# Performance work log

Hardware: AMD Instinct MI355X
Metric: run time of the kernel (lower is better)

## Reference

```python
import jax, jax.numpy as jnp
import numpy as np

B, S, D = 64, 4096, 64          # bsz*n_heads, seq_len, head_size
WINDOW = 256                    # num_toks_attended
NEG = -10000.0


def setup_inputs() -> dict:
    key = jax.random.key(0)
    kq, kk, kv = jax.random.split(key, 3)
    q = jax.random.normal(kq, (B, S, D), dtype=jnp.float32)
    k = jax.random.normal(kk, (B, S, D), dtype=jnp.float32)
    v = jax.random.normal(kv, (B, S, D), dtype=jnp.float32)
    return {"q": q, "k": k, "v": v}


def reference(q, k, v):
    # sliding_window_attn, topk_for_softmax=-1 (plain softmax)
    b, s, d = q.shape
    hw = WINDOW // 2                       # half window = 128
    n = s // hw                            # number of half-window bins
    split = lambda x: x.reshape(b, n, hw, d)
    bq, bk, bv = split(q), split(k), split(v)

    def cat_half_neighbours(x):
        # left-rolled, self, right-rolled half-bins -> [b, n, 3*hw, d]
        return jnp.concatenate(
            (jnp.roll(x, 1, axis=1), x, jnp.roll(x, -1, axis=1)), axis=-2)

    bk = cat_half_neighbours(bk)
    bv = cat_half_neighbours(bv)

    dots = jnp.einsum('bnid,bnjd->bnij', bq, bk) * (d ** -0.5)  # [b,n,hw,3hw]

    # mask: strict lower triangle on left block, none on middle,
    # upper-incl-diagonal on right block (as in the torch code)
    lmask = jnp.tril(jnp.ones((hw, hw), dtype=bool), -1)
    mask = jnp.concatenate((lmask, jnp.zeros_like(lmask), ~lmask), axis=-1)
    dots = jnp.where(mask, NEG, dots)

    p = jax.nn.softmax(dots, axis=-1)
    bo = jnp.einsum('bnij,bnjd->bnid', p, bv)
    return bo.reshape(b, s, d)
```

## Files before the change

kernel.cpp:

```cpp
#include <hip/hip_runtime.h>
#include <hip/hip_bf16.h>
#include <stdint.h>

using f32x4  = __attribute__((ext_vector_type(4))) float;
using bf16x8 = __attribute__((ext_vector_type(8))) __bf16;
using bf16x2 = __attribute__((ext_vector_type(2))) __bf16;
typedef unsigned int u32;

#define SEQ  4096
#define NEGV -10000.0f

__global__ __launch_bounds__(256) void lattn_kern(
        const float* __restrict__ Q, const float* __restrict__ K,
        const float* __restrict__ V, float* __restrict__ O)
{
    __shared__ __bf16 Kl[320 * 64];
    __shared__ __bf16 Vt[64 * 320];

    const int tid  = threadIdx.x;
    const int wv   = tid >> 6;
    const int lane = tid & 63;
    const int g    = lane >> 4;
    const int c    = lane & 15;

    const int obid = blockIdx.x;
    const int bid  = (obid & 7) * 512 + (obid >> 3);
    const int b    = bid >> 6;
    const int tb   = bid & 63;
    const int t0   = tb * 64;

    const size_t baseB = (size_t)b * (SEQ * 64);

    #pragma unroll
    for (int i = 0; i < 10; ++i) {
        const int ch   = tid + i * 256;
        const int row  = ch >> 3;
        const int dg   = ch & 7;
        const int grow = (t0 - 128 + row) & (SEQ - 1);
        const float* src = K + baseB + (size_t)grow * 64 + dg * 8;
        f32x4 k0 = *(const f32x4*)(src);
        f32x4 k1 = *(const f32x4*)(src + 4);
        bf16x8 hk;
        #pragma unroll
        for (int u = 0; u < 4; ++u) { hk[u] = (__bf16)k0[u]; hk[u + 4] = (__bf16)k1[u]; }
        const u32 kb = (u32)row * 128u + (u32)((dg ^ (row & 7)) * 16);
        *(bf16x8*)((char*)Kl + kb) = hk;
    }

    #pragma unroll
    for (int i = 0; i < 5; ++i) {
        const int ch   = tid + i * 256;
        const int rp   = ch >> 3;
        const int dg   = ch & 7;
        const int grow = (t0 - 128 + 2 * rp) & (SEQ - 1);
        const float* src = V + baseB + (size_t)grow * 64 + dg * 8;
        f32x4 a0 = *(const f32x4*)(src);
        f32x4 a1 = *(const f32x4*)(src + 4);
        f32x4 b0 = *(const f32x4*)(src + 64);
        f32x4 b1 = *(const f32x4*)(src + 68);
        #pragma unroll
        for (int u = 0; u < 8; ++u) {
            const int d  = dg * 8 + u;
            const float lo = (u < 4) ? a0[u] : a1[u - 4];
            const float hi = (u < 4) ? b0[u] : b1[u - 4];
            bf16x2 pv; pv[0] = (__bf16)lo; pv[1] = (__bf16)hi;
            const u32 sw = (u32)(u ^ dg);
            const u32 vb = ((u32)d * 640u + (u32)rp * 4u) ^ (sw << 4);
            *(bf16x2*)((char*)Vt + vb) = pv;
        }
    }

    bf16x8 aq[2];
    {
        const float* qp = Q + baseB + (size_t)(t0 + wv * 16 + c) * 64 + g * 8;
        #pragma unroll
        for (int kk = 0; kk < 2; ++kk) {
            f32x4 q0 = *(const f32x4*)(qp + kk * 32);
            f32x4 q1 = *(const f32x4*)(qp + kk * 32 + 4);
            #pragma unroll
            for (int u = 0; u < 4; ++u) { aq[kk][u] = (__bf16)q0[u]; aq[kk][u + 4] = (__bf16)q1[u]; }
        }
    }

    __syncthreads();

    f32x4 s_[20];
    #pragma unroll
    for (int t = 0; t < 20; ++t) {
        if (t >= wv && t <= wv + 16) {
            const u32 key = (u32)(t * 16 + c);
            const u32 sw  = key & 7u;
            const u32 ka  = key * 128u;
            bf16x8 kb0 = *(const bf16x8*)((const char*)Kl + ka + (((u32)g ^ sw) << 4));
            bf16x8 kb1 = *(const bf16x8*)((const char*)Kl + ka + (((u32)(g + 4) ^ sw) << 4));
            f32x4 acc = {0.f, 0.f, 0.f, 0.f};
            __builtin_amdgcn_s_setprio(1);
            acc = __builtin_amdgcn_mfma_f32_16x16x32_bf16(aq[0], kb0, acc, 0, 0, 0);
            acc = __builtin_amdgcn_mfma_f32_16x16x32_bf16(aq[1], kb1, acc, 0, 0, 0);
            __builtin_amdgcn_s_setprio(0);
            s_[t] = acc;
        } else {
            s_[t] = (f32x4){0.f, 0.f, 0.f, 0.f};
        }
    }

    const int i0 = wv * 16 + g * 4;
    float mx[4] = {-3e38f, -3e38f, -3e38f, -3e38f};
    #pragma unroll
    for (int t = 0; t < 20; ++t) {
        if (t >= wv && t <= wv + 16) {
            const int j = t * 16 + c;
            #pragma unroll
            for (int r = 0; r < 4; ++r) {
                const int iq = i0 + r;
                float val = s_[t][r] * 0.125f;
                val = (j < iq || j >= iq + 256) ? NEGV : val;
                s_[t][r] = val;
                mx[r] = fmaxf(mx[r], val);
            }
        }
    }
    #pragma unroll
    for (int d = 1; d < 16; d <<= 1) {
        #pragma unroll
        for (int r = 0; r < 4; ++r) mx[r] = fmaxf(mx[r], __shfl_xor(mx[r], d, 64));
    }
    float sm[4] = {0.f, 0.f, 0.f, 0.f};
    #pragma unroll
    for (int t = 0; t < 20; ++t) {
        if (t >= wv && t <= wv + 16) {
            #pragma unroll
            for (int r = 0; r < 4; ++r) {
                float p = __expf(s_[t][r] - mx[r]);
                s_[t][r] = p; sm[r] += p;
            }
        }
    }
    #pragma unroll
    for (int d = 1; d < 16; d <<= 1) {
        #pragma unroll
        for (int r = 0; r < 4; ++r) sm[r] += __shfl_xor(sm[r], d, 64);
    }
    float inv[4];
    #pragma unroll
    for (int r = 0; r < 4; ++r) inv[r] = 1.0f / sm[r];

    __syncthreads();

    f32x4 o[4] = {{0,0,0,0},{0,0,0,0},{0,0,0,0},{0,0,0,0}};
    __bf16* Pw = Kl + wv * 1024;
    #pragma unroll
    for (int c5 = 0; c5 < 5; ++c5) {
        #pragma unroll
        for (int tt = 0; tt < 4; ++tt) {
            const int t = c5 * 4 + tt;
            #pragma unroll
            for (int r = 0; r < 4; ++r) {
                const int prow = g * 4 + r;
                const u32 pb = ((u32)prow * 128u + (u32)(tt * 16 + c) * 2u)
                             ^ ((u32)(prow & 7) << 4);
                *(__bf16*)((char*)Pw + pb) = (__bf16)(s_[t][r] * inv[r]);
            }
        }
        #pragma unroll
        for (int kk = 0; kk < 2; ++kk) {
            const u32 pa_b = ((u32)c * 128u + (u32)(kk * 64 + g * 16))
                           ^ ((u32)(c & 7) << 4);
            const bf16x8 pa = *(const bf16x8*)((const char*)Pw + pa_b);
            const int key0 = c5 * 64 + kk * 32 + g * 8;
            __builtin_amdgcn_s_setprio(1);
            #pragma unroll
            for (int dt = 0; dt < 4; ++dt) {
                const int d  = dt * 16 + c;
                const u32 sw = (u32)((d & 7) ^ ((d >> 3) & 7));
                const u32 vb = ((u32)d * 640u + (u32)key0 * 2u) ^ (sw << 4);
                const bf16x8 bb = *(const bf16x8*)((const char*)Vt + vb);
                o[dt] = __builtin_amdgcn_mfma_f32_16x16x32_bf16(pa, bb, o[dt], 0, 0, 0);
            }
            __builtin_amdgcn_s_setprio(0);
        }
    }

    #pragma unroll
    for (int dt = 0; dt < 4; ++dt) {
        #pragma unroll
        for (int r = 0; r < 4; ++r) {
            const int row = t0 + wv * 16 + g * 4 + r;
            O[baseB + (size_t)row * 64 + dt * 16 + c] = o[dt][r];
        }
    }
}

extern "C" void kernel_launch(void* const* d_in, const int* in_sizes, int n_in,
                              void* d_out, int out_size, void* d_ws, size_t ws_size,
                              hipStream_t stream) {
    const float* q = (const float*)d_in[0];
    const float* k = (const float*)d_in[1];
    const float* v = (const float*)d_in[2];
    float* o = (float*)d_out;
    const int nB = in_sizes[0] / (SEQ * 64);
    dim3 grid(nB * 64), block(256);
    hipLaunchKernelGGL(lattn_kern, grid, block, 0, stream, q, k, v, o);
}
```

Measured before the change: 84.92 us.

## Make blocks persistent over eight query tiles with a rolling K/V ring buffer

Each block now handles 512 consecutive queries in eight 64-row steps instead of one 64-row tile. K and V stay in a 320-row circular shared buffer, and each step loads and converts only the 64 new rows, with the global loads issued early to overlap compute. This removes the 5x redundant K/V halo loading and conversion of the old one-tile-per-block scheme. The softmax also drops the max subtraction and applies the masking and normalisation after the PV product, which risks overflow on large logits. Grid size shrinks eightfold to 512 blocks, which lowers parallelism and adds more barriers per block.

```diff
diff --git a/kernel.cpp b/kernel.cpp
--- a/kernel.cpp
+++ b/kernel.cpp
@@ -7,10 +7,9 @@
 using bf16x2 = __attribute__((ext_vector_type(2))) __bf16;
 typedef unsigned int u32;
 
-#define SEQ  4096
-#define NEGV -10000.0f
-
-__global__ __launch_bounds__(256) void lattn_kern(
+#define SEQ 4096
+
+__global__ __launch_bounds__(256, 2) void lattn_kern(
         const float* __restrict__ Q, const float* __restrict__ K,
         const float* __restrict__ V, float* __restrict__ O)
 {
@@ -23,170 +22,195 @@
     const int g    = lane >> 4;
     const int c    = lane & 15;
 
-    const int obid = blockIdx.x;
-    const int bid  = (obid & 7) * 512 + (obid >> 3);
-    const int b    = bid >> 6;
-    const int tb   = bid & 63;
-    const int t0   = tb * 64;
-
+    const int b    = blockIdx.x >> 3;
+    const int oct  = blockIdx.x & 7;
     const size_t baseB = (size_t)b * (SEQ * 64);
+    const int t00  = oct * 512;
+
+    int r0 = (t00 + SEQ - 128) % 320;
 
     #pragma unroll
-    for (int i = 0; i < 10; ++i) {
-        const int ch   = tid + i * 256;
-        const int row  = ch >> 3;
-        const int dg   = ch & 7;
-        const int grow = (t0 - 128 + row) & (SEQ - 1);
+    for (int it = 0; it < 10; ++it) {
+        const int ch = tid + it * 256;
+        const int j = ch >> 3, dg = ch & 7;
+        const int grow = (t00 - 128 + j) & (SEQ - 1);
+        int row = r0 + j; if (row >= 320) row -= 320;
         const float* src = K + baseB + (size_t)grow * 64 + dg * 8;
-        f32x4 k0 = *(const f32x4*)(src);
-        f32x4 k1 = *(const f32x4*)(src + 4);
+        f32x4 k0 = *(const f32x4*)src, k1 = *(const f32x4*)(src + 4);
         bf16x8 hk;
         #pragma unroll
         for (int u = 0; u < 4; ++u) { hk[u] = (__bf16)k0[u]; hk[u + 4] = (__bf16)k1[u]; }
-        const u32 kb = (u32)row * 128u + (u32)((dg ^ (row & 7)) * 16);
-        *(bf16x8*)((char*)Kl + kb) = hk;
-    }
-
-    #pragma unroll
-    for (int i = 0; i < 5; ++i) {
-        const int ch   = tid + i * 256;
-        const int rp   = ch >> 3;
-        const int dg   = ch & 7;
-        const int grow = (t0 - 128 + 2 * rp) & (SEQ - 1);
-        const float* src = V + baseB + (size_t)grow * 64 + dg * 8;
-        f32x4 a0 = *(const f32x4*)(src);
-        f32x4 a1 = *(const f32x4*)(src + 4);
-        f32x4 b0 = *(const f32x4*)(src + 64);
-        f32x4 b1 = *(const f32x4*)(src + 68);
-        #pragma unroll
-        for (int u = 0; u < 8; ++u) {
-            const int d  = dg * 8 + u;
-            const float lo = (u < 4) ? a0[u] : a1[u - 4];
-            const float hi = (u < 4) ? b0[u] : b1[u - 4];
-            bf16x2 pv; pv[0] = (__bf16)lo; pv[1] = (__bf16)hi;
-            const u32 sw = (u32)(u ^ dg);
-            const u32 vb = ((u32)d * 640u + (u32)rp * 4u) ^ (sw << 4);
-            *(bf16x2*)((char*)Vt + vb) = pv;
-        }
-    }
-
-    bf16x8 aq[2];
-    {
-        const float* qp = Q + baseB + (size_t)(t0 + wv * 16 + c) * 64 + g * 8;
-        #pragma unroll
-        for (int kk = 0; kk < 2; ++kk) {
-            f32x4 q0 = *(const f32x4*)(qp + kk * 32);
-            f32x4 q1 = *(const f32x4*)(qp + kk * 32 + 4);
-            #pragma unroll
-            for (int u = 0; u < 4; ++u) { aq[kk][u] = (__bf16)q0[u]; aq[kk][u + 4] = (__bf16)q1[u]; }
-        }
-    }
-
-    __syncthreads();
-
-    f32x4 s_[20];
-    #pragma unroll
-    for (int t = 0; t < 20; ++t) {
-        if (t >= wv && t <= wv + 16) {
-            const u32 key = (u32)(t * 16 + c);
-            const u32 sw  = key & 7u;
-            const u32 ka  = key * 128u;
-            bf16x8 kb0 = *(const bf16x8*)((const char*)Kl + ka + (((u32)g ^ sw) << 4));
-            bf16x8 kb1 = *(const bf16x8*)((const char*)Kl + ka + (((u32)(g + 4) ^ sw) << 4));
-            f32x4 acc = {0.f, 0.f, 0.f, 0.f};
-            __builtin_amdgcn_s_setprio(1);
-            acc = __builtin_amdgcn_mfma_f32_16x16x32_bf16(aq[0], kb0, acc, 0, 0, 0);
-            acc = __builtin_amdgcn_mfma_f32_16x16x32_bf16(aq[1], kb1, acc, 0, 0, 0);
-            __builtin_amdgcn_s_setprio(0);
-            s_[t] = acc;
-        } else {
-            s_[t] = (f32x4){0.f, 0.f, 0.f, 0.f};
-        }
-    }
-
-    const int i0 = wv * 16 + g * 4;
-    float mx[4] = {-3e38f, -3e38f, -3e38f, -3e38f};
-    #pragma unroll
-    for (int t = 0; t < 20; ++t) {
-        if (t >= wv && t <= wv + 16) {
-            const int j = t * 16 + c;
-            #pragma unroll
-            for (int r = 0; r < 4; ++r) {
-                const int iq = i0 + r;
-                float val = s_[t][r] * 0.125f;
-                val = (j < iq || j >= iq + 256) ? NEGV : val;
-                s_[t][r] = val;
-                mx[r] = fmaxf(mx[r], val);
-            }
-        }
+        *(bf16x8*)((char*)Kl + row * 128 + (((u32)dg ^ (u32)(row & 7)) << 4)) = hk;
     }
     #pragma unroll
-    for (int d = 1; d < 16; d <<= 1) {
-        #pragma unroll
-        for (int r = 0; r < 4; ++r) mx[r] = fmaxf(mx[r], __shfl_xor(mx[r], d, 64));
+    for (int it = 0; it < 5; ++it) {
+        const int ch = tid + it * 256;
+        const int rp = ch >> 3, dg = ch & 7;
+        const int grow = (t00 - 128 + 2 * rp) & (SEQ - 1);
+        int col = r0 + 2 * rp; if (col >= 320) col -= 320;
+        const float* src = V + baseB + (size_t)grow * 64 + dg * 8;
+        f32x4 a0 = *(const f32x4*)src,        a1 = *(const f32x4*)(src + 4);
+        f32x4 b0 = *(const f32x4*)(src + 64), b1 = *(const f32x4*)(src + 68);
+        #pragma unroll
+        for (int u = 0; u < 8; ++u) {
+            const int d = dg * 8 + u;
+            bf16x2 pv;
+            pv[0] = (__bf16)((u < 4) ? a0[u] : a1[u - 4]);
+            pv[1] = (__bf16)((u < 4) ? b0[u] : b1[u - 4]);
+            const u32 sw = (u32)(u ^ dg);
+            *(bf16x2*)((char*)Vt + (((u32)d * 640u + (u32)col * 2u) ^ (sw << 4))) = pv;
+        }
     }
-    float sm[4] = {0.f, 0.f, 0.f, 0.f};
-    #pragma unroll
-    for (int t = 0; t < 20; ++t) {
-        if (t >= wv && t <= wv + 16) {
+
+    const u32 swc = (u32)(c & 7);
+
+    for (int i = 0; i < 8; ++i) {
+        const int t0 = t00 + i * 64;
+        __syncthreads();
+
+        f32x4 dk[4], dv[4];
+        int krow0 = 0, krow1 = 0, vcol = 0, kdg = 0, vdg = 0;
+        if (i < 7) {
+            {
+                const int jj = tid >> 3; kdg = tid & 7;
+                const int grow0 = (t0 + 192 + jj) & (SEQ - 1);
+                const float* s0 = K + baseB + (size_t)grow0 * 64 + kdg * 8;
+                dk[0] = *(const f32x4*)s0; dk[1] = *(const f32x4*)(s0 + 4);
+                krow0 = r0 + jj;
+                const int grow1 = (t0 + 192 + jj + 32) & (SEQ - 1);
+                const float* s1 = K + baseB + (size_t)grow1 * 64 + kdg * 8;
+                dk[2] = *(const f32x4*)s1; dk[3] = *(const f32x4*)(s1 + 4);
+                krow1 = r0 + jj + 32;
+            }
+            {
+                const int rp = tid >> 3; vdg = tid & 7;
+                const int grow = (t0 + 192 + 2 * rp) & (SEQ - 1);
+                const float* s0 = V + baseB + (size_t)grow * 64 + vdg * 8;
+                dv[0] = *(const f32x4*)s0;        dv[1] = *(const f32x4*)(s0 + 4);
+                dv[2] = *(const f32x4*)(s0 + 64); dv[3] = *(const f32x4*)(s0 + 68);
+                vcol = r0 + 2 * rp;
+            }
+        }
+
+        bf16x8 aq0, aq1;
+        {
+            const float* qp = Q + baseB + (size_t)(t0 + wv * 16 + c) * 64 + g * 8;
+            f32x4 q0 = *(const f32x4*)qp,        q1 = *(const f32x4*)(qp + 4);
+            f32x4 q2 = *(const f32x4*)(qp + 32), q3 = *(const f32x4*)(qp + 36);
+            #pragma unroll
+            for (int u = 0; u < 4; ++u) {
+                aq0[u] = (__bf16)q0[u]; aq0[u + 4] = (__bf16)q1[u];
+                aq1[u] = (__bf16)q2[u]; aq1[u + 4] = (__bf16)q3[u];
+            }
+        }
+
+        f32x4 s_[20];
+        const int rc = r0 + c;
+        #pragma unroll
+        for (int t = 0; t < 20; ++t) {
+            if (t >= wv && t <= wv + 16) {
+                int row = rc + 16 * t; if (row >= 320) row -= 320;
+                const u32 ka = (u32)row * 128u;
+                bf16x8 kb0 = *(const bf16x8*)((const char*)Kl + ka + (((u32)g ^ swc) << 4));
+                bf16x8 kb1 = *(const bf16x8*)((const char*)Kl + ka + (((u32)(g + 4) ^ swc) << 4));
+                f32x4 acc = {0.f, 0.f, 0.f, 0.f};
+                __builtin_amdgcn_s_setprio(1);
+                acc = __builtin_amdgcn_mfma_f32_16x16x32_bf16(aq0, kb0, acc, 0, 0, 0);
+                acc = __builtin_amdgcn_mfma_f32_16x16x32_bf16(aq1, kb1, acc, 0, 0, 0);
+                __builtin_amdgcn_s_setprio(0);
+                s_[t] = acc;
+            } else {
+                s_[t] = (f32x4){0.f, 0.f, 0.f, 0.f};
+            }
+        }
+        __syncthreads();
+
+        float sm4[4] = {0.f, 0.f, 0.f, 0.f};
+        #pragma unroll
+        for (int t = 0; t < 20; ++t) {
+            if (t >= wv && t <= wv + 16) {
+                #pragma unroll
+                for (int r = 0; r < 4; ++r) {
+                    float e = __expf(s_[t][r] * 0.125f);
+                    if (t == wv)      e = (c <  g * 4 + r) ? 0.f : e;
+                    if (t == wv + 16) e = (c >= g * 4 + r) ? 0.f : e;
+                    s_[t][r] = e; sm4[r] += e;
+                }
+            }
+        }
+        #pragma unroll
+        for (int d = 1; d < 16; d <<= 1) {
+            #pragma unroll
+            for (int r = 0; r < 4; ++r) sm4[r] += __shfl_xor(sm4[r], d, 64);
+        }
+        float inv[4];
+        #pragma unroll
+        for (int r = 0; r < 4; ++r) inv[r] = 1.0f / sm4[r];
+
+        char* Pw = (char*)Kl + r0 * 128 + wv * 2048;
+        f32x4 o[4] = {{0,0,0,0},{0,0,0,0},{0,0,0,0},{0,0,0,0}};
+        #pragma unroll
+        for (int c5 = 0; c5 < 5; ++c5) {
+            #pragma unroll
+            for (int tt = 0; tt < 4; ++tt) {
+                const int t = c5 * 4 + tt;
+                const bool live = (t >= wv && t <= wv + 16);
+                #pragma unroll
+                for (int r = 0; r < 4; ++r) {
+                    const int prow = g * 4 + r;
+                    const u32 pb = ((u32)prow * 128u + (u32)(tt * 16 + c) * 2u)
+                                 ^ ((u32)(prow & 7) << 4);
+                    float pv_ = live ? s_[t][r] : 0.f;
+                    *(__bf16*)(Pw + pb) = (__bf16)pv_;
+                }
+            }
+            #pragma unroll
+            for (int kk = 0; kk < 2; ++kk) {
+                const u32 pa_b = ((u32)c * 128u + (u32)(kk * 64 + g * 16)) ^ (swc << 4);
+                const bf16x8 pa = *(const bf16x8*)(Pw + pa_b);
+                int col0 = r0 + c5 * 64 + kk * 32 + g * 8;
+                if (col0 >= 320) col0 -= 320;
+                __builtin_amdgcn_s_setprio(1);
+                #pragma unroll
+                for (int dt = 0; dt < 4; ++dt) {
+                    const int d  = dt * 16 + c;
+                    const u32 sw = (u32)((d & 7) ^ ((d >> 3) & 7));
+                    const u32 vb = ((u32)d * 640u + (u32)col0 * 2u) ^ (sw << 4);
+                    const bf16x8 bb = *(const bf16x8*)((const char*)Vt + vb);
+                    o[dt] = __builtin_amdgcn_mfma_f32_16x16x32_bf16(pa, bb, o[dt], 0, 0, 0);
+                }
+                __builtin_amdgcn_s_setprio(0);
+            }
+        }
+
+        #pragma unroll
+        for (int dt = 0; dt < 4; ++dt) {
             #pragma unroll
             for (int r = 0; r < 4; ++r) {
-                float p = __expf(s_[t][r] - mx[r]);
-                s_[t][r] = p; sm[r] += p;
-            }
-        }
-    }
-    #pragma unroll
-    for (int d = 1; d < 16; d <<= 1) {
-        #pragma unroll
-        for (int r = 0; r < 4; ++r) sm[r] += __shfl_xor(sm[r], d, 64);
-    }
-    float inv[4];
-    #pragma unroll
-    for (int r = 0; r < 4; ++r) inv[r] = 1.0f / sm[r];
-
-    __syncthreads();
-
-    f32x4 o[4] = {{0,0,0,0},{0,0,0,0},{0,0,0,0},{0,0,0,0}};
-    __bf16* Pw = Kl + wv * 1024;
-    #pragma unroll
-    for (int c5 = 0; c5 < 5; ++c5) {
-        #pragma unroll
-        for (int tt = 0; tt < 4; ++tt) {
-            const int t = c5 * 4 + tt;
-            #pragma unroll
-            for (int r = 0; r < 4; ++r) {
-                const int prow = g * 4 + r;
-                const u32 pb = ((u32)prow * 128u + (u32)(tt * 16 + c) * 2u)
-                             ^ ((u32)(prow & 7) << 4);
-                *(__bf16*)((char*)Pw + pb) = (__bf16)(s_[t][r] * inv[r]);
-            }
-        }
-        #pragma unroll
-        for (int kk = 0; kk < 2; ++kk) {
-            const u32 pa_b = ((u32)c * 128u + (u32)(kk * 64 + g * 16))
-                           ^ ((u32)(c & 7) << 4);
-            const bf16x8 pa = *(const bf16x8*)((const char*)Pw + pa_b);
-            const int key0 = c5 * 64 + kk * 32 + g * 8;
-            __builtin_amdgcn_s_setprio(1);
-            #pragma unroll
-            for (int dt = 0; dt < 4; ++dt) {
-                const int d  = dt * 16 + c;
-                const u32 sw = (u32)((d & 7) ^ ((d >> 3) & 7));
-                const u32 vb = ((u32)d * 640u + (u32)key0 * 2u) ^ (sw << 4);
-                const bf16x8 bb = *(const bf16x8*)((const char*)Vt + vb);
-                o[dt] = __builtin_amdgcn_mfma_f32_16x16x32_bf16(pa, bb, o[dt], 0, 0, 0);
-            }
-            __builtin_amdgcn_s_setprio(0);
-        }
-    }
-
-    #pragma unroll
-    for (int dt = 0; dt < 4; ++dt) {
-        #pragma unroll
-        for (int r = 0; r < 4; ++r) {
-            const int row = t0 + wv * 16 + g * 4 + r;
-            O[baseB + (size_t)row * 64 + dt * 16 + c] = o[dt][r];
+                const int row = t0 + wv * 16 + g * 4 + r;
+                O[baseB + (size_t)row * 64 + dt * 16 + c] = o[dt][r] * inv[r];
+            }
+        }
+
+        if (i < 7) {
+            __syncthreads();
+            bf16x8 hk;
+            #pragma unroll
+            for (int u = 0; u < 4; ++u) { hk[u] = (__bf16)dk[0][u]; hk[u + 4] = (__bf16)dk[1][u]; }
+            *(bf16x8*)((char*)Kl + krow0 * 128 + (((u32)kdg ^ (u32)(krow0 & 7)) << 4)) = hk;
+            #pragma unroll
+            for (int u = 0; u < 4; ++u) { hk[u] = (__bf16)dk[2][u]; hk[u + 4] = (__bf16)dk[3][u]; }
+            *(bf16x8*)((char*)Kl + krow1 * 128 + (((u32)kdg ^ (u32)(krow1 & 7)) << 4)) = hk;
+            #pragma unroll
+            for (int u = 0; u < 8; ++u) {
+                const int d = vdg * 8 + u;
+                bf16x2 pv;
+                pv[0] = (__bf16)((u < 4) ? dv[0][u] : dv[1][u - 4]);
+                pv[1] = (__bf16)((u < 4) ? dv[2][u] : dv[3][u - 4]);
+                const u32 sw = (u32)(u ^ vdg);
+                *(bf16x2*)((char*)Vt + (((u32)d * 640u + (u32)vcol * 2u) ^ (sw << 4))) = pv;
+            }
+            r0 += 64; if (r0 >= 320) r0 -= 320;
         }
     }
 }
@@ -199,6 +223,6 @@
     const float* v = (const float*)d_in[2];
     float* o = (float*)d_out;
     const int nB = in_sizes[0] / (SEQ * 64);
-    dim3 grid(nB * 64), block(256);
+    dim3 grid(nB * 8), block(256);
     hipLaunchKernelGGL(lattn_kern, grid, block, 0, stream, q, k, v, o);
 }
```

Measured after the change: 83.94 us. No clear change (-1.1%).
